# Optimization experiments

Measured on AMD Instinct MI355X. Metric: run time of the kernel, lower is better.

Reference implementation:

```python
import math
import jax, jax.numpy as jnp
import numpy as np

NUM_HEADS = 8
GROUPS = 32
EPS = 1e-5

def group_norm(x, w, b):
    # x: [B, C, H, W], GroupNorm with 32 groups, biased variance (matches torch)
    B, C, H, W = x.shape
    xg = x.reshape(B, GROUPS, C // GROUPS, H, W)
    mu = xg.mean(axis=(2, 3, 4), keepdims=True)
    var = xg.var(axis=(2, 3, 4), keepdims=True)
    xn = ((xg - mu) * jax.lax.rsqrt(var + EPS)).reshape(B, C, H, W)
    return xn * w[None, :, None, None] + b[None, :, None, None]

def setup_inputs() -> dict:
    key = jax.random.key(0)
    ks = jax.random.split(key, 3)
    B, C, H, W = 8, 512, 32, 32
    x = jax.random.normal(ks[0], (B, C, H, W), dtype=jnp.float32)
    norm_w = jnp.ones((C,), jnp.float32)
    norm_b = jnp.zeros((C,), jnp.float32)
    qkv_w = jax.random.normal(ks[1], (3 * C, C), dtype=jnp.float32) * (1.0 / math.sqrt(C))
    qkv_b = jnp.zeros((3 * C,), jnp.float32)
    proj_w = jax.random.normal(ks[2], (C, C), dtype=jnp.float32) * (1.0 / math.sqrt(C))
    proj_b = jnp.zeros((C,), jnp.float32)
    return {"x": x, "norm_w": norm_w, "norm_b": norm_b,
            "qkv_w": qkv_w, "qkv_b": qkv_b, "proj_w": proj_w, "proj_b": proj_b}

def reference(x, norm_w, norm_b, qkv_w, qkv_b, proj_w, proj_b):
    B, C, H, W = x.shape
    T = H * W
    heads = NUM_HEADS
    ch = C // heads  # head dim

    # norm + 1x1 conv producing packed qkv: [B, 3C, T]
    xn = group_norm(x, norm_w, norm_b)
    qkv = jnp.einsum('oc,bchw->bohw', qkv_w, xn).reshape(B, 3 * C, T) + qkv_b[None, :, None]

    # QKVAttentionLegacy: reshape to [B*heads, 3*ch, T], split q/k/v per head
    qkv = qkv.reshape(B * heads, 3 * ch, T)
    q, k, v = jnp.split(qkv, 3, axis=1)  # each [B*heads, ch, T]
    scale = 1.0 / math.sqrt(math.sqrt(ch))
    w = jnp.einsum('bct,bcs->bts', q * scale, k * scale)  # [B*heads, T, T]
    w = jax.nn.softmax(w.astype(jnp.float32), axis=-1).astype(qkv.dtype)
    a = jnp.einsum('bts,bcs->bct', w, v)  # [B*heads, ch, T]
    h = a.reshape(B, C, H, W)

    # proj_out 1x1 conv + residual
    h = jnp.einsum('oc,bchw->bohw', proj_w, h) + proj_b[None, :, None, None]
    return x + h
```

## Files before the change

### kernel.cpp

```cpp
#include <hip/hip_runtime.h>
#include <stdint.h>


typedef float  f32x4  __attribute__((ext_vector_type(4)));
typedef short  s16x4  __attribute__((ext_vector_type(4)));
typedef short  s16x8  __attribute__((ext_vector_type(8)));
typedef __bf16 bf16x8 __attribute__((ext_vector_type(8)));

#define QK_SCALE 0.4246609f

__device__ __forceinline__ f32x4 mfma_bf16_16x16x32(s16x8 a, s16x8 b, f32x4 c){
  return __builtin_amdgcn_mfma_f32_16x16x32_bf16(
      __builtin_bit_cast(bf16x8, a), __builtin_bit_cast(bf16x8, b), c, 0, 0, 0);
}

__device__ __forceinline__ short f2bf(float v){
  return __builtin_bit_cast(short, static_cast<__bf16>(v));
}

__device__ __forceinline__ void gload16(const void* g, void* l){
  __builtin_amdgcn_global_load_lds(
      (const __attribute__((address_space(1))) void*)g,
      (__attribute__((address_space(3))) void*)l, 16, 0, 0);
}

__global__ __launch_bounds__(256) void gn_fused_kernel(const float* __restrict__ x,
    const float* __restrict__ w, const float* __restrict__ bia,
    short* __restrict__ xnT, const float* __restrict__ qkv_w,
    const float* __restrict__ proj_w, short* __restrict__ qwb,
    short* __restrict__ pwb){
  const int tid = threadIdx.x;
  if (blockIdx.x < 256){
    __shared__ float ssw[4], sqw[4];
    __shared__ float scs[16], shs[16];
    __shared__ short L[16*1032];
    const int bg = blockIdx.x;
    const int b = bg >> 5, g = bg & 31;
    const float* xb = x + (size_t)bg * 16384;
    float4 v[16];
    float s = 0.f, q = 0.f;
    #pragma unroll
    for (int i = 0; i < 16; ++i){
      v[i] = ((const float4*)xb)[tid + i*256];
      s += v[i].x + v[i].y + v[i].z + v[i].w;
      q += v[i].x*v[i].x + v[i].y*v[i].y + v[i].z*v[i].z + v[i].w*v[i].w;
    }
    #pragma unroll
    for (int off = 32; off > 0; off >>= 1){
      s += __shfl_xor(s, off, 64);
      q += __shfl_xor(q, off, 64);
    }
    if ((tid & 63) == 0){ ssw[tid >> 6] = s; sqw[tid >> 6] = q; }
    __syncthreads();
    if (tid < 16){
      const float st = (ssw[0] + ssw[1]) + (ssw[2] + ssw[3]);
      const float qt = (sqw[0] + sqw[1]) + (sqw[2] + sqw[3]);
      const float mu  = st * (1.f/16384.f);
      const float var = qt * (1.f/16384.f) - mu*mu;
      const float rstd = rsqrtf(var + 1e-5f);
      const int ch = g*16 + tid;
      const float sc = rstd * w[ch];
      scs[tid] = sc;
      shs[tid] = bia[ch] - mu * sc;
    }
    __syncthreads();
    #pragma unroll
    for (int i = 0; i < 16; ++i){
      const float sc = scs[i], sh = shs[i];
      s16x4 o;
      o[0]=f2bf(v[i].x*sc+sh); o[1]=f2bf(v[i].y*sc+sh);
      o[2]=f2bf(v[i].z*sc+sh); o[3]=f2bf(v[i].w*sc+sh);
      *(s16x4*)&L[i*1032 + tid*4] = o;
    }
    __syncthreads();
    short* ob = xnT + (size_t)b * 524288 + g*16;
    #pragma unroll
    for (int u = 0; u < 8; ++u){
      const int unit = tid + u*256;
      const int t = unit >> 1, c8 = (unit & 1)*8;
      s16x8 o;
      #pragma unroll
      for (int j = 0; j < 8; ++j) o[j] = L[(c8 + j)*1032 + t];
      *(s16x8*)(ob + (size_t)t*512 + c8) = o;
    }
  } else {
    const int i = (blockIdx.x - 256)*256 + tid;
    const float* in; short* out; float s;
    if (i < 98304){
      in = qkv_w + (size_t)i*8; out = qwb + (size_t)i*8;
      s = (((i >> 6) % 192) < 128) ? QK_SCALE : 1.f;
    } else {
      const int j = i - 98304;
      in = proj_w + (size_t)j*8; out = pwb + (size_t)j*8;
      s = 1.f;
    }
    const float4* p = (const float4*)in;
    float4 a = p[0], b2 = p[1];
    s16x8 o;
    o[0]=f2bf(a.x*s);  o[1]=f2bf(a.y*s);  o[2]=f2bf(a.z*s);  o[3]=f2bf(a.w*s);
    o[4]=f2bf(b2.x*s); o[5]=f2bf(b2.y*s); o[6]=f2bf(b2.z*s); o[7]=f2bf(b2.w*s);
    *(s16x8*)out = o;
  }
}

template<int MODE, int NB>
__global__ __launch_bounds__(256) void gemm_k512(const short* __restrict__ W,
    const short* __restrict__ act, const float* __restrict__ bias,
    const float* __restrict__ resid, void* __restrict__ outp,
    void* __restrict__ outp2, void* __restrict__ outp3){
  constexpr int NSF = NB / 32;
  constexpr int SMEM_BYTES = (MODE == 2) ? 34816 : 32768;
  const int b  = blockIdx.x;
  const int tid  = threadIdx.x;
  const int lane = tid & 63, w = tid >> 6;
  const int wm = w >> 1, wn = w & 1;
  const int lm = lane & 15, lb = lane >> 4;
  const int xr = (lm >> 1) & 3;

  int part, m0, n0;
  if constexpr (MODE == 0){
    const int z = blockIdx.z;
    part = z >> 2;
    if (part < 2){ m0 = (z & 3)*128; n0 = blockIdx.y*128; }
    else         { m0 = blockIdx.y*128; n0 = 1024 + (z & 3)*128; }
  } else {
    part = 0; m0 = blockIdx.y*128; n0 = blockIdx.z*NB;
  }

  __shared__ __align__(16) char smem[SMEM_BYTES];
  short* Asb = (short*)smem;
  short* Bsb = (short*)(smem + 16384);

  const short* actb = act + (size_t)b * 524288;

  auto arow = [&](int r) -> const short* {
    if constexpr (MODE == 0){
      if (part < 2){
        const int m = m0 + r;
        return W + (size_t)(192*(m>>6) + part*64 + (m&63)) * 512;
      }
      return actb + (size_t)(m0 + r) * 512;
    } else {
      return W + (size_t)(m0 + r) * 512;
    }
  };
  auto brow = [&](int r) -> const short* {
    if constexpr (MODE == 0){
      if (part < 2) return actb + (size_t)(n0 + r) * 512;
      const int o = n0 + r;
      return W + (size_t)(192*((o>>6)&7) + 128 + (o&63)) * 512;
    } else {
      return actb + (size_t)(n0 + r) * 512;
    }
  };

  auto stage = [&](int t, int buf){
    const int k0 = t * 32;
    #pragma unroll
    for (int i = 0; i < 2; ++i){
      const int c = tid + i*256;
      const int r = c >> 2, sj = (c & 3) ^ ((c >> 3) & 3);
      gload16(arow(r) + k0 + sj*8, Asb + buf*4096 + (c>>2)*32 + (c&3)*8);
    }
    #pragma unroll
    for (int i = 0; i < NB/64; ++i){
      const int c = tid + i*256;
      const int r = c >> 2, sj = (c & 3) ^ ((c >> 3) & 3);
      gload16(brow(r) + k0 + sj*8, Bsb + buf*(NB*32) + (c>>2)*32 + (c&3)*8);
    }
  };

  f32x4 acc[4][NSF] = {};
  stage(0, 0);

  for (int t = 0; t < 16; ++t){
    __syncthreads();
    if (t + 1 < 16) stage(t + 1, (t + 1) & 1);
    const int buf = t & 1;

    s16x8 af[4], bfr[NSF];
    #pragma unroll
    for (int ms = 0; ms < 4; ++ms){
      const int row = wm*64 + ms*16 + lm;
      af[ms] = *(const s16x8*)(Asb + buf*4096 + row*32 + ((lb ^ xr) << 3));
    }
    #pragma unroll
    for (int ns = 0; ns < NSF; ++ns){
      const int row = wn*(NB/2) + ns*16 + lm;
      bfr[ns] = *(const s16x8*)(Bsb + buf*(NB*32) + row*32 + ((lb ^ xr) << 3));
    }
    #pragma unroll
    for (int ns = 0; ns < NSF; ++ns)
      #pragma unroll
      for (int ms = 0; ms < 4; ++ms)
        acc[ms][ns] = mfma_bf16_16x16x32(af[ms], bfr[ns], acc[ms][ns]);
  }

  const int mo = m0 + wm*64, no = n0 + wn*(NB/2);
  if constexpr (MODE == 0){
    if (part < 2){
      short* outT = (short*)(part == 0 ? outp : outp2) + (size_t)b * 524288;
      const int hh = m0/64 + wm;
      float bm[16];
      #pragma unroll
      for (int ms = 0; ms < 4; ++ms)
        #pragma unroll
        for (int r = 0; r < 4; ++r){
          const int m = mo + ms*16 + 4*lb + r;
          bm[ms*4+r] = QK_SCALE * bias[192*(m>>6) + part*64 + (m&63)];
        }
      #pragma unroll
      for (int ms = 0; ms < 4; ++ms)
        #pragma unroll
        for (int ns = 0; ns < NSF; ++ns){
          const int n = no + ns*16 + lm;
          const size_t a = ((size_t)hh*128 + (n>>4)*2 + (ms>>1))*512
                         + (((ms*2 + (lb>>1)) & 3)*16 + (n&15))*8 + 4*(lb&1);
          s16x4 o;
          #pragma unroll
          for (int r = 0; r < 4; ++r) o[r] = f2bf(acc[ms][ns][r] + bm[ms*4+r]);
          *(s16x4*)(outT + a) = o;
        }
    } else {
      short* vout = (short*)outp3 + (size_t)b * 524288;
      float bn[NSF];
      #pragma unroll
      for (int ns = 0; ns < NSF; ++ns){
        const int o = no + ns*16 + lm;
        bn[ns] = bias[192*((o>>6)&7) + 128 + (o&63)];
      }
      #pragma unroll
      for (int ms = 0; ms < 4; ++ms)
        #pragma unroll
        for (int ns = 0; ns < NSF; ++ns){
          const int m = mo + ms*16 + 4*lb;
          const int n = no + ns*16 + lm;
          const int h = (n >> 6) & 7, c = n & 63;
          const size_t a = ((size_t)h*128 + (c>>4)*32 + (m>>5))*512
                         + (((m>>2)&3)*16 + (c&15))*8 + ((m>>4)&1)*4;
          s16x4 o;
          #pragma unroll
          for (int r = 0; r < 4; ++r) o[r] = f2bf(acc[ms][ns][r] + bn[ns]);
          *(s16x4*)(vout + a) = o;
        }
    }
  } else {
    const float* xr2 = resid + (size_t)b * 524288;
    float4 rv[8];
    #pragma unroll
    for (int p = 0; p < 8; ++p){
      const int row = p*16 + (tid >> 4);
      rv[p] = *(const float4*)(xr2 + (size_t)(m0 + row)*1024 + n0 + (tid & 15)*4);
    }
    __syncthreads();
    float* Lf = (float*)smem;
    #pragma unroll
    for (int ms = 0; ms < 4; ++ms)
      #pragma unroll
      for (int ns = 0; ns < NSF; ++ns)
        #pragma unroll
        for (int r = 0; r < 4; ++r)
          Lf[(wm*64 + ms*16 + 4*lb + r)*68 + wn*32 + ns*16 + lm] = acc[ms][ns][r];
    __syncthreads();
    float* out = (float*)outp + (size_t)b * 524288;
    #pragma unroll
    for (int p = 0; p < 8; ++p){
      const int row = p*16 + (tid >> 4);
      const int c4  = (tid & 15) * 4;
      float4 v = *(const float4*)&Lf[row*68 + c4];
      const float bs = bias[m0 + row];
      const size_t off = (size_t)(m0 + row)*1024 + n0 + c4;
      float4 ov = make_float4(v.x+bs+rv[p].x, v.y+bs+rv[p].y,
                              v.z+bs+rv[p].z, v.w+bs+rv[p].w);
      *(float4*)(out + off) = ov;
    }
  }
}

__global__ __launch_bounds__(512) void attn13_kernel(const short* __restrict__ qbuf,
    const short* __restrict__ kbuf, const short* __restrict__ vbuf,
    short* __restrict__ attT){
  const int bid = blockIdx.x;
  const int bh = bid & 63, tc = bid >> 6;
  const int b = bh >> 3, h = bh & 7;
  const int tid = threadIdx.x;
  const int lane = tid & 63, w = tid >> 6;
  const int lm = lane & 15, lb = lane >> 4;
  const int t0 = tc * 256;

  const short* qb = qbuf + (size_t)b*524288 + (size_t)h*65536 + lane*8;
  const short* kb = kbuf + (size_t)b*524288 + (size_t)h*65536 + lane*8;
  const short* vb = vbuf + (size_t)b*524288 + (size_t)h*65536 + lane*8;

  __shared__ short Tl[256*72];

  s16x8 qf[2][2];
  #pragma unroll
  for (int tb = 0; tb < 2; ++tb)
    #pragma unroll
    for (int ks = 0; ks < 2; ++ks)
      qf[tb][ks] = *(const s16x8*)(qb +
          (size_t)((((t0 >> 4) + w*2 + tb)*2) + ks)*512);

  f32x4 of[2][4] = {};
  f32x4 lacc[2] = {};
  s16x8 kA[2][4], kB[2][4], vA[2][4], vB[2][4];

  auto load_k = [&](int it, s16x8 (&kf)[2][4]){
    #pragma unroll
    for (int ks = 0; ks < 2; ++ks)
      #pragma unroll
      for (int ms = 0; ms < 4; ++ms)
        kf[ks][ms] = *(const s16x8*)(kb + (size_t)((it*4 + ms)*2 + ks)*512);
  };
  auto load_v = [&](int it, s16x8 (&vf)[2][4]){
    #pragma unroll
    for (int ks2 = 0; ks2 < 2; ++ks2)
      #pragma unroll
      for (int cs = 0; cs < 4; ++cs)
        vf[ks2][cs] = *(const s16x8*)(vb + (size_t)(cs*32 + it*2 + ks2)*512);
  };

  auto body = [&](int it, s16x8 (&kcur)[2][4], s16x8 (&vcur)[2][4],
                  s16x8 (&knxt)[2][4], s16x8 (&vnxt)[2][4]){
    if (it + 1 < 16){ load_k(it + 1, knxt); load_v(it + 1, vnxt); }

    f32x4 sf[2][4];
    #pragma unroll
    for (int tb = 0; tb < 2; ++tb)
      #pragma unroll
      for (int ms = 0; ms < 4; ++ms) sf[tb][ms] = 0.f;
    #pragma unroll
    for (int ks = 0; ks < 2; ++ks)
      #pragma unroll
      for (int ms = 0; ms < 4; ++ms){
        sf[0][ms] = mfma_bf16_16x16x32(kcur[ks][ms], qf[0][ks], sf[0][ms]);
        sf[1][ms] = mfma_bf16_16x16x32(kcur[ks][ms], qf[1][ks], sf[1][ms]);
      }

    s16x8 pbf[2][2];
    #pragma unroll
    for (int tb = 0; tb < 2; ++tb)
      #pragma unroll
      for (int ms = 0; ms < 4; ++ms)
        #pragma unroll
        for (int r = 0; r < 4; ++r){
          const float e = __builtin_amdgcn_exp2f(sf[tb][ms][r]);
          lacc[tb][r] += e;
          pbf[tb][ms >> 1][(ms & 1)*4 + r] = f2bf(e);
        }

    #pragma unroll
    for (int ks2 = 0; ks2 < 2; ++ks2)
      #pragma unroll
      for (int cs = 0; cs < 4; ++cs){
        of[0][cs] = mfma_bf16_16x16x32(vcur[ks2][cs], pbf[0][ks2], of[0][cs]);
        of[1][cs] = mfma_bf16_16x16x32(vcur[ks2][cs], pbf[1][ks2], of[1][cs]);
      }
  };

  load_k(0, kA);
  load_v(0, vA);
  for (int it2 = 0; it2 < 16; it2 += 2){
    body(it2,     kA, vA, kB, vB);
    body(it2 + 1, kB, vB, kA, vA);
  }

  float lsum[2];
  #pragma unroll
  for (int tb = 0; tb < 2; ++tb){
    lsum[tb] = (lacc[tb][0] + lacc[tb][1]) + (lacc[tb][2] + lacc[tb][3]);
    lsum[tb] += __shfl_xor(lsum[tb], 16, 64);
    lsum[tb] += __shfl_xor(lsum[tb], 32, 64);
  }
  const float inv0 = 1.f / lsum[0], inv1 = 1.f / lsum[1];

  #pragma unroll
  for (int tb = 0; tb < 2; ++tb)
    #pragma unroll
    for (int cs = 0; cs < 4; ++cs){
      s16x4 o;
      #pragma unroll
      for (int r = 0; r < 4; ++r)
        o[r] = f2bf(of[tb][cs][r] * (tb ? inv1 : inv0));
      *(s16x4*)&Tl[(w*32 + tb*16 + lm)*72 + cs*16 + 4*lb] = o;
    }
  __syncthreads();
  short* outb = attT + (size_t)b*524288 + (size_t)t0*512 + h*64;
  #pragma unroll
  for (int i = 0; i < 4; ++i){
    const int g = tid + i*512, r = g >> 3, c8 = g & 7;
    *(uint4*)(outb + (size_t)r*512 + c8*8) = *(const uint4*)&Tl[r*72 + c8*8];
  }
}

extern "C" void kernel_launch(void* const* d_in, const int* in_sizes, int n_in,
                              void* d_out, int out_size, void* d_ws, size_t ws_size,
                              hipStream_t stream){
  const float* x      = (const float*)d_in[0];
  const float* norm_w = (const float*)d_in[1];
  const float* norm_b = (const float*)d_in[2];
  const float* qkv_w  = (const float*)d_in[3];
  const float* qkv_b  = (const float*)d_in[4];
  const float* proj_w = (const float*)d_in[5];
  const float* proj_b = (const float*)d_in[6];

  char* ws = (char*)d_ws;
  short*  xnT   = (short*)(ws + 4096);
  short*  qwb   = (short*)(ws + 8392704);
  short*  pwb   = (short*)(ws + 9965568);
  short*  qbuf  = (short*)(ws + 10489856);
  short*  kbuf  = (short*)(ws + 18878464);
  short*  vbuf  = (short*)(ws + 27267072);
  short*  attT  = (short*)(ws + 35655680);

  gn_fused_kernel<<<dim3(768), dim3(256), 0, stream>>>(x, norm_w, norm_b, xnT,
      qkv_w, proj_w, qwb, pwb);
  gemm_k512<0,128><<<dim3(8, 8, 12), dim3(256), 0, stream>>>(qwb, xnT, qkv_b, nullptr,
      (void*)qbuf, (void*)kbuf, (void*)vbuf);
  attn13_kernel<<<dim3(256), dim3(512), 0, stream>>>(qbuf, kbuf, vbuf, attT);
  gemm_k512<2,64><<<dim3(8, 4, 16), dim3(256), 0, stream>>>(pwb, attT, proj_b, x,
      d_out, nullptr, nullptr);
}
```

Measured before the change: 68.11 us.

## Pre-tile GEMM operands into MFMA fragment layout and drop LDS staging

The producers (groupnorm, weight conversion, attention output) now write their bf16 outputs in a fragment-tiled layout, 16-row by 32-k tiles of 512 elements. Each lane can then load its MFMA operand with one contiguous 16-byte global read. The QKV and projection GEMMs drop the LDS double-buffered global_load_lds staging and barriers and read fragments directly from global memory, relying on cache for reuse across waves. This removes the LDS traffic and synchronisation cost. In exchange, global and L2 reads go up because operands are no longer shared through LDS, and there is no software prefetch of the next k-step.

Result: slower. 78.71 us (+15.6%).

```diff
diff --git a/kernel.cpp b/kernel.cpp
--- a/kernel.cpp
+++ b/kernel.cpp
@@ -16,12 +16,6 @@
 
 __device__ __forceinline__ short f2bf(float v){
   return __builtin_bit_cast(short, static_cast<__bf16>(v));
-}
-
-__device__ __forceinline__ void gload16(const void* g, void* l){
-  __builtin_amdgcn_global_load_lds(
-      (const __attribute__((address_space(1))) void*)g,
-      (__attribute__((address_space(3))) void*)l, 16, 0, 0);
 }
 
 __global__ __launch_bounds__(256) void gn_fused_kernel(const float* __restrict__ x,
@@ -73,207 +67,198 @@
       *(s16x4*)&L[i*1032 + tid*4] = o;
     }
     __syncthreads();
-    short* ob = xnT + (size_t)b * 524288 + g*16;
+    short* ob = xnT + (size_t)b * 524288;
     #pragma unroll
     for (int u = 0; u < 8; ++u){
       const int unit = tid + u*256;
-      const int t = unit >> 1, c8 = (unit & 1)*8;
+      const int t = unit >> 1, u1 = unit & 1;
       s16x8 o;
       #pragma unroll
-      for (int j = 0; j < 8; ++j) o[j] = L[(c8 + j)*1032 + t];
-      *(s16x8*)(ob + (size_t)t*512 + c8) = o;
+      for (int j = 0; j < 8; ++j) o[j] = L[(u1*8 + j)*1032 + t];
+      const size_t a = (size_t)(((t>>4)*16 + (g>>1))*512
+                     + (t&15)*8 + (((g*2 + u1)) & 3)*128);
+      *(s16x8*)(ob + a) = o;
     }
   } else {
     const int i = (blockIdx.x - 256)*256 + tid;
-    const float* in; short* out; float s;
     if (i < 98304){
-      in = qkv_w + (size_t)i*8; out = qwb + (size_t)i*8;
-      s = (((i >> 6) % 192) < 128) ? QK_SCALE : 1.f;
+      const int wr = i >> 6, cin0 = (i & 63)*8;
+      const int h = wr / 192, within = wr - h*192;
+      const int p = within >> 6, c = h*64 + (within & 63);
+      const float s = (p < 2) ? QK_SCALE : 1.f;
+      const float4* pp = (const float4*)(qkv_w + (size_t)i*8);
+      float4 a = pp[0], b2 = pp[1];
+      s16x8 o;
+      o[0]=f2bf(a.x*s);  o[1]=f2bf(a.y*s);  o[2]=f2bf(a.z*s);  o[3]=f2bf(a.w*s);
+      o[4]=f2bf(b2.x*s); o[5]=f2bf(b2.y*s); o[6]=f2bf(b2.z*s); o[7]=f2bf(b2.w*s);
+      const size_t ad = (size_t)p*262144 + ((c>>4)*16 + (cin0>>5))*512
+                      + (c&15)*8 + ((cin0>>3)&3)*128;
+      *(s16x8*)(qwb + ad) = o;
     } else {
-      const int j = i - 98304;
-      in = proj_w + (size_t)j*8; out = pwb + (size_t)j*8;
-      s = 1.f;
-    }
-    const float4* p = (const float4*)in;
-    float4 a = p[0], b2 = p[1];
-    s16x8 o;
-    o[0]=f2bf(a.x*s);  o[1]=f2bf(a.y*s);  o[2]=f2bf(a.z*s);  o[3]=f2bf(a.w*s);
-    o[4]=f2bf(b2.x*s); o[5]=f2bf(b2.y*s); o[6]=f2bf(b2.z*s); o[7]=f2bf(b2.w*s);
-    *(s16x8*)out = o;
-  }
-}
-
-template<int MODE, int NB>
-__global__ __launch_bounds__(256) void gemm_k512(const short* __restrict__ W,
-    const short* __restrict__ act, const float* __restrict__ bias,
-    const float* __restrict__ resid, void* __restrict__ outp,
-    void* __restrict__ outp2, void* __restrict__ outp3){
-  constexpr int NSF = NB / 32;
-  constexpr int SMEM_BYTES = (MODE == 2) ? 34816 : 32768;
-  const int b  = blockIdx.x;
-  const int tid  = threadIdx.x;
+      const int j2 = i - 98304;
+      const int o_r = j2 >> 6, cin0 = (j2 & 63)*8;
+      const float4* pp = (const float4*)(proj_w + (size_t)j2*8);
+      float4 a = pp[0], b2 = pp[1];
+      s16x8 o;
+      o[0]=f2bf(a.x);  o[1]=f2bf(a.y);  o[2]=f2bf(a.z);  o[3]=f2bf(a.w);
+      o[4]=f2bf(b2.x); o[5]=f2bf(b2.y); o[6]=f2bf(b2.z); o[7]=f2bf(b2.w);
+      const size_t ad = (size_t)((o_r>>4)*16 + (cin0>>5))*512
+                      + (o_r&15)*8 + ((cin0>>3)&3)*128;
+      *(s16x8*)(pwb + ad) = o;
+    }
+  }
+}
+
+__global__ __launch_bounds__(256) void gemm_qkv_kernel(const short* __restrict__ qwb,
+    const short* __restrict__ xnT, const float* __restrict__ bias,
+    short* __restrict__ qbuf, short* __restrict__ kbuf, short* __restrict__ vbuf){
+  const int b = blockIdx.x, y = blockIdx.y, z = blockIdx.z;
+  const int part = z >> 2;
+  const int tid = threadIdx.x;
   const int lane = tid & 63, w = tid >> 6;
   const int wm = w >> 1, wn = w & 1;
   const int lm = lane & 15, lb = lane >> 4;
-  const int xr = (lm >> 1) & 3;
-
-  int part, m0, n0;
-  if constexpr (MODE == 0){
-    const int z = blockIdx.z;
-    part = z >> 2;
-    if (part < 2){ m0 = (z & 3)*128; n0 = blockIdx.y*128; }
-    else         { m0 = blockIdx.y*128; n0 = 1024 + (z & 3)*128; }
+
+  const short* xb = xnT + (size_t)b * 524288;
+  int m0, n0; const short *Abase, *Bbase;
+  if (part < 2){ m0 = (z & 3)*128; n0 = y*128;
+                 Abase = qwb + (size_t)part*262144; Bbase = xb; }
+  else         { m0 = y*128; n0 = (z & 3)*128;
+                 Abase = xb; Bbase = qwb + (size_t)2*262144; }
+
+  const short* Ab = Abase + lane*8;
+  const short* Bb = Bbase + lane*8;
+  const int at0 = (m0 >> 4) + wm*4;
+  const int bt0 = (n0 >> 4) + wn*4;
+
+  f32x4 acc[4][4] = {};
+  #pragma unroll
+  for (int kk = 0; kk < 16; ++kk){
+    s16x8 af[4], bf[4];
+    #pragma unroll
+    for (int ms = 0; ms < 4; ++ms)
+      af[ms] = *(const s16x8*)(Ab + (size_t)(((at0 + ms)*16 + kk))*512);
+    #pragma unroll
+    for (int ns = 0; ns < 4; ++ns)
+      bf[ns] = *(const s16x8*)(Bb + (size_t)(((bt0 + ns)*16 + kk))*512);
+    #pragma unroll
+    for (int ns = 0; ns < 4; ++ns)
+      #pragma unroll
+      for (int ms = 0; ms < 4; ++ms)
+        acc[ms][ns] = mfma_bf16_16x16x32(af[ms], bf[ns], acc[ms][ns]);
+  }
+
+  const int mo = m0 + wm*64, no = n0 + wn*64;
+  if (part < 2){
+    short* outT = (part == 0 ? qbuf : kbuf) + (size_t)b * 524288;
+    const int hh = m0/64 + wm;
+    float bm[16];
+    #pragma unroll
+    for (int ms = 0; ms < 4; ++ms)
+      #pragma unroll
+      for (int r = 0; r < 4; ++r){
+        const int m = mo + ms*16 + 4*lb + r;
+        bm[ms*4+r] = QK_SCALE * bias[192*(m>>6) + part*64 + (m&63)];
+      }
+    #pragma unroll
+    for (int ms = 0; ms < 4; ++ms)
+      #pragma unroll
+      for (int ns = 0; ns < 4; ++ns){
+        const int n = no + ns*16 + lm;
+        const size_t a = ((size_t)hh*128 + (n>>4)*2 + (ms>>1))*512
+                       + (((ms*2 + (lb>>1)) & 3)*16 + (n&15))*8 + 4*(lb&1);
+        s16x4 o;
+        #pragma unroll
+        for (int r = 0; r < 4; ++r) o[r] = f2bf(acc[ms][ns][r] + bm[ms*4+r]);
+        *(s16x4*)(outT + a) = o;
+      }
   } else {
-    part = 0; m0 = blockIdx.y*128; n0 = blockIdx.z*NB;
-  }
-
-  __shared__ __align__(16) char smem[SMEM_BYTES];
-  short* Asb = (short*)smem;
-  short* Bsb = (short*)(smem + 16384);
-
-  const short* actb = act + (size_t)b * 524288;
-
-  auto arow = [&](int r) -> const short* {
-    if constexpr (MODE == 0){
-      if (part < 2){
-        const int m = m0 + r;
-        return W + (size_t)(192*(m>>6) + part*64 + (m&63)) * 512;
+    short* vout = vbuf + (size_t)b * 524288;
+    float bn[4];
+    #pragma unroll
+    for (int ns = 0; ns < 4; ++ns){
+      const int o = no + ns*16 + lm;
+      bn[ns] = bias[192*(o>>6) + 128 + (o&63)];
+    }
+    #pragma unroll
+    for (int ms = 0; ms < 4; ++ms)
+      #pragma unroll
+      for (int ns = 0; ns < 4; ++ns){
+        const int m = mo + ms*16 + 4*lb;
+        const int n = no + ns*16 + lm;
+        const int h = n >> 6, c = n & 63;
+        const size_t a = ((size_t)h*128 + (c>>4)*32 + (m>>5))*512
+                       + (((m>>2)&3)*16 + (c&15))*8 + ((m>>4)&1)*4;
+        s16x4 o;
+        #pragma unroll
+        for (int r = 0; r < 4; ++r) o[r] = f2bf(acc[ms][ns][r] + bn[ns]);
+        *(s16x4*)(vout + a) = o;
       }
-      return actb + (size_t)(m0 + r) * 512;
-    } else {
-      return W + (size_t)(m0 + r) * 512;
-    }
-  };
-  auto brow = [&](int r) -> const short* {
-    if constexpr (MODE == 0){
-      if (part < 2) return actb + (size_t)(n0 + r) * 512;
-      const int o = n0 + r;
-      return W + (size_t)(192*((o>>6)&7) + 128 + (o&63)) * 512;
-    } else {
-      return actb + (size_t)(n0 + r) * 512;
-    }
-  };
-
-  auto stage = [&](int t, int buf){
-    const int k0 = t * 32;
-    #pragma unroll
-    for (int i = 0; i < 2; ++i){
-      const int c = tid + i*256;
-      const int r = c >> 2, sj = (c & 3) ^ ((c >> 3) & 3);
-      gload16(arow(r) + k0 + sj*8, Asb + buf*4096 + (c>>2)*32 + (c&3)*8);
-    }
-    #pragma unroll
-    for (int i = 0; i < NB/64; ++i){
-      const int c = tid + i*256;
-      const int r = c >> 2, sj = (c & 3) ^ ((c >> 3) & 3);
-      gload16(brow(r) + k0 + sj*8, Bsb + buf*(NB*32) + (c>>2)*32 + (c&3)*8);
-    }
-  };
-
-  f32x4 acc[4][NSF] = {};
-  stage(0, 0);
-
-  for (int t = 0; t < 16; ++t){
-    __syncthreads();
-    if (t + 1 < 16) stage(t + 1, (t + 1) & 1);
-    const int buf = t & 1;
-
-    s16x8 af[4], bfr[NSF];
-    #pragma unroll
-    for (int ms = 0; ms < 4; ++ms){
-      const int row = wm*64 + ms*16 + lm;
-      af[ms] = *(const s16x8*)(Asb + buf*4096 + row*32 + ((lb ^ xr) << 3));
-    }
-    #pragma unroll
-    for (int ns = 0; ns < NSF; ++ns){
-      const int row = wn*(NB/2) + ns*16 + lm;
-      bfr[ns] = *(const s16x8*)(Bsb + buf*(NB*32) + row*32 + ((lb ^ xr) << 3));
-    }
-    #pragma unroll
-    for (int ns = 0; ns < NSF; ++ns)
+  }
+}
+
+__global__ __launch_bounds__(256) void gemm_proj_kernel(const short* __restrict__ pwb,
+    const short* __restrict__ attT, const float* __restrict__ bias,
+    const float* __restrict__ resid, float* __restrict__ outp){
+  const int b = blockIdx.x;
+  const int m0 = blockIdx.y * 128;
+  const int n0 = blockIdx.z * 64;
+  const int tid = threadIdx.x;
+  const int lane = tid & 63, w = tid >> 6;
+  const int wm = w >> 1, wn = w & 1;
+  const int lm = lane & 15, lb = lane >> 4;
+
+  __shared__ __align__(16) float Lf[128*68];
+
+  const short* Ab = pwb + lane*8;
+  const short* Bb = attT + (size_t)b * 524288 + lane*8;
+  const int at0 = (m0 >> 4) + wm*4;
+  const int bt0 = (n0 >> 4) + wn*2;
+
+  f32x4 acc[4][2] = {};
+  #pragma unroll
+  for (int kk = 0; kk < 16; ++kk){
+    s16x8 af[4], bf[2];
+    #pragma unroll
+    for (int ms = 0; ms < 4; ++ms)
+      af[ms] = *(const s16x8*)(Ab + (size_t)(((at0 + ms)*16 + kk))*512);
+    #pragma unroll
+    for (int ns = 0; ns < 2; ++ns)
+      bf[ns] = *(const s16x8*)(Bb + (size_t)(((bt0 + ns)*16 + kk))*512);
+    #pragma unroll
+    for (int ns = 0; ns < 2; ++ns)
       #pragma unroll
       for (int ms = 0; ms < 4; ++ms)
-        acc[ms][ns] = mfma_bf16_16x16x32(af[ms], bfr[ns], acc[ms][ns]);
-  }
-
-  const int mo = m0 + wm*64, no = n0 + wn*(NB/2);
-  if constexpr (MODE == 0){
-    if (part < 2){
-      short* outT = (short*)(part == 0 ? outp : outp2) + (size_t)b * 524288;
-      const int hh = m0/64 + wm;
-      float bm[16];
-      #pragma unroll
-      for (int ms = 0; ms < 4; ++ms)
-        #pragma unroll
-        for (int r = 0; r < 4; ++r){
-          const int m = mo + ms*16 + 4*lb + r;
-          bm[ms*4+r] = QK_SCALE * bias[192*(m>>6) + part*64 + (m&63)];
-        }
-      #pragma unroll
-      for (int ms = 0; ms < 4; ++ms)
-        #pragma unroll
-        for (int ns = 0; ns < NSF; ++ns){
-          const int n = no + ns*16 + lm;
-          const size_t a = ((size_t)hh*128 + (n>>4)*2 + (ms>>1))*512
-                         + (((ms*2 + (lb>>1)) & 3)*16 + (n&15))*8 + 4*(lb&1);
-          s16x4 o;
-          #pragma unroll
-          for (int r = 0; r < 4; ++r) o[r] = f2bf(acc[ms][ns][r] + bm[ms*4+r]);
-          *(s16x4*)(outT + a) = o;
-        }
-    } else {
-      short* vout = (short*)outp3 + (size_t)b * 524288;
-      float bn[NSF];
-      #pragma unroll
-      for (int ns = 0; ns < NSF; ++ns){
-        const int o = no + ns*16 + lm;
-        bn[ns] = bias[192*((o>>6)&7) + 128 + (o&63)];
-      }
-      #pragma unroll
-      for (int ms = 0; ms < 4; ++ms)
-        #pragma unroll
-        for (int ns = 0; ns < NSF; ++ns){
-          const int m = mo + ms*16 + 4*lb;
-          const int n = no + ns*16 + lm;
-          const int h = (n >> 6) & 7, c = n & 63;
-          const size_t a = ((size_t)h*128 + (c>>4)*32 + (m>>5))*512
-                         + (((m>>2)&3)*16 + (c&15))*8 + ((m>>4)&1)*4;
-          s16x4 o;
-          #pragma unroll
-          for (int r = 0; r < 4; ++r) o[r] = f2bf(acc[ms][ns][r] + bn[ns]);
-          *(s16x4*)(vout + a) = o;
-        }
-    }
-  } else {
-    const float* xr2 = resid + (size_t)b * 524288;
-    float4 rv[8];
-    #pragma unroll
-    for (int p = 0; p < 8; ++p){
-      const int row = p*16 + (tid >> 4);
-      rv[p] = *(const float4*)(xr2 + (size_t)(m0 + row)*1024 + n0 + (tid & 15)*4);
-    }
-    __syncthreads();
-    float* Lf = (float*)smem;
-    #pragma unroll
-    for (int ms = 0; ms < 4; ++ms)
-      #pragma unroll
-      for (int ns = 0; ns < NSF; ++ns)
-        #pragma unroll
-        for (int r = 0; r < 4; ++r)
-          Lf[(wm*64 + ms*16 + 4*lb + r)*68 + wn*32 + ns*16 + lm] = acc[ms][ns][r];
-    __syncthreads();
-    float* out = (float*)outp + (size_t)b * 524288;
-    #pragma unroll
-    for (int p = 0; p < 8; ++p){
-      const int row = p*16 + (tid >> 4);
-      const int c4  = (tid & 15) * 4;
-      float4 v = *(const float4*)&Lf[row*68 + c4];
-      const float bs = bias[m0 + row];
-      const size_t off = (size_t)(m0 + row)*1024 + n0 + c4;
-      float4 ov = make_float4(v.x+bs+rv[p].x, v.y+bs+rv[p].y,
-                              v.z+bs+rv[p].z, v.w+bs+rv[p].w);
-      *(float4*)(out + off) = ov;
-    }
+        acc[ms][ns] = mfma_bf16_16x16x32(af[ms], bf[ns], acc[ms][ns]);
+  }
+
+  const float* xr2 = resid + (size_t)b * 524288;
+  float4 rv[8];
+  #pragma unroll
+  for (int p = 0; p < 8; ++p){
+    const int row = p*16 + (tid >> 4);
+    rv[p] = *(const float4*)(xr2 + (size_t)(m0 + row)*1024 + n0 + (tid & 15)*4);
+  }
+
+  #pragma unroll
+  for (int ms = 0; ms < 4; ++ms)
+    #pragma unroll
+    for (int ns = 0; ns < 2; ++ns)
+      #pragma unroll
+      for (int r = 0; r < 4; ++r)
+        Lf[(wm*64 + ms*16 + 4*lb + r)*68 + wn*32 + ns*16 + lm] = acc[ms][ns][r];
+  __syncthreads();
+  float* out = outp + (size_t)b * 524288;
+  #pragma unroll
+  for (int p = 0; p < 8; ++p){
+    const int row = p*16 + (tid >> 4);
+    const int c4  = (tid & 15) * 4;
+    float4 v = *(const float4*)&Lf[row*68 + c4];
+    const float bs = bias[m0 + row];
+    const size_t off = (size_t)(m0 + row)*1024 + n0 + c4;
+    float4 ov = make_float4(v.x+bs+rv[p].x, v.y+bs+rv[p].y,
+                            v.z+bs+rv[p].z, v.w+bs+rv[p].w);
+    *(float4*)(out + off) = ov;
   }
 }
 
@@ -324,7 +309,6 @@
   auto body = [&](int it, s16x8 (&kcur)[2][4], s16x8 (&vcur)[2][4],
                   s16x8 (&knxt)[2][4], s16x8 (&vnxt)[2][4]){
     if (it + 1 < 16){ load_k(it + 1, knxt); load_v(it + 1, vnxt); }
-
     f32x4 sf[2][4];
     #pragma unroll
     for (int tb = 0; tb < 2; ++tb)
@@ -337,7 +321,6 @@
         sf[0][ms] = mfma_bf16_16x16x32(kcur[ks][ms], qf[0][ks], sf[0][ms]);
         sf[1][ms] = mfma_bf16_16x16x32(kcur[ks][ms], qf[1][ks], sf[1][ms]);
       }
-
     s16x8 pbf[2][2];
     #pragma unroll
     for (int tb = 0; tb < 2; ++tb)
@@ -349,7 +332,6 @@
           lacc[tb][r] += e;
           pbf[tb][ms >> 1][(ms & 1)*4 + r] = f2bf(e);
         }
-
     #pragma unroll
     for (int ks2 = 0; ks2 < 2; ++ks2)
       #pragma unroll
@@ -386,11 +368,14 @@
       *(s16x4*)&Tl[(w*32 + tb*16 + lm)*72 + cs*16 + 4*lb] = o;
     }
   __syncthreads();
-  short* outb = attT + (size_t)b*524288 + (size_t)t0*512 + h*64;
+  short* ab = attT + (size_t)b*524288;
   #pragma unroll
   for (int i = 0; i < 4; ++i){
-    const int g = tid + i*512, r = g >> 3, c8 = g & 7;
-    *(uint4*)(outb + (size_t)r*512 + c8*8) = *(const uint4*)&Tl[r*72 + c8*8];
+    const int gidx = tid + i*512, r = gidx >> 3, c8 = gidx & 7;
+    const int tg = t0 + r;
+    const size_t a = (size_t)(((tg>>4)*16 + h*2 + (c8>>2))*512
+                   + (tg&15)*8 + (c8&3)*128);
+    *(uint4*)(ab + a) = *(const uint4*)&Tl[r*72 + c8*8];
   }
 }
 
@@ -416,9 +401,9 @@
 
   gn_fused_kernel<<<dim3(768), dim3(256), 0, stream>>>(x, norm_w, norm_b, xnT,
       qkv_w, proj_w, qwb, pwb);
-  gemm_k512<0,128><<<dim3(8, 8, 12), dim3(256), 0, stream>>>(qwb, xnT, qkv_b, nullptr,
-      (void*)qbuf, (void*)kbuf, (void*)vbuf);
+  gemm_qkv_kernel<<<dim3(8, 8, 12), dim3(256), 0, stream>>>(qwb, xnT, qkv_b,
+      qbuf, kbuf, vbuf);
   attn13_kernel<<<dim3(256), dim3(512), 0, stream>>>(qbuf, kbuf, vbuf, attT);
-  gemm_k512<2,64><<<dim3(8, 4, 16), dim3(256), 0, stream>>>(pwb, attT, proj_b, x,
-      d_out, nullptr, nullptr);
-}
+  gemm_proj_kernel<<<dim3(8, 4, 16), dim3(256), 0, stream>>>(pwb, attT, proj_b,
+      x, (float*)d_out);
+}
```
